# Kernel tuning notes

Measured on AMD Instinct MI355X. Metric: run time of the kernel, lower is better.

## Reference

```python
import jax, jax.numpy as jnp
import numpy as np
from jax import lax

B, CX, CZ, H, W = 8, 96, 96, 256, 256
HEADS = 4


def conv2d(x, w, groups=1, pad=0):
    return lax.conv_general_dilated(
        x, w, window_strides=(1, 1), padding=[(pad, pad), (pad, pad)],
        dimension_numbers=('NCHW', 'OIHW', 'NCHW'),
        feature_group_count=groups)


def setup_inputs() -> dict:
    key = jax.random.key(0)
    ks = jax.random.split(key, 8)
    def init_w(k, shape):
        fan_in = shape[1] * shape[2] * shape[3]
        bound = 1.0 / np.sqrt(fan_in)
        return jax.random.uniform(k, shape, jnp.float32, -bound, bound)
    return {
        'x': jax.random.normal(ks[0], (B, CX, H, W), jnp.float32),
        'z': jax.random.normal(ks[1], (B, CZ, H, W), jnp.float32),
        'kv_w1': init_w(ks[2], (2 * CZ, CZ, 1, 1)),
        'kv_w2': init_w(ks[3], (2 * CZ, 2, 3, 3)),   # grouped: groups=CZ, 2 in-ch per group
        'q_w1': init_w(ks[4], (CX, CX, 1, 1)),
        'q_w2': init_w(ks[5], (CX, 1, 3, 3)),        # depthwise: groups=CX
        'proj_w': init_w(ks[6], (CX, CX, 1, 1)),
        'temperature': jnp.ones((HEADS, 1, 1), jnp.float32),
    }


def _forward(x, z, kv_w1, kv_w2, q_w1, q_w2, proj_w, temperature):
    b, cx, h, w = x.shape
    cz = z.shape[1]
    hw = h * w
    kv = conv2d(conv2d(z, kv_w1), kv_w2, groups=cz, pad=1)   # [b, 2cz, h, w]
    q = conv2d(conv2d(x, q_w1), q_w2, groups=cx, pad=1)      # [b, cx, h, w]
    k, v = jnp.split(kv, 2, axis=1)
    # b (head c) h w -> b head c (h w)
    q = q.reshape(b, HEADS, cx // HEADS, hw)
    k = k.reshape(b, HEADS, cz // HEADS, hw)
    v = v.reshape(b, HEADS, cz // HEADS, hw)
    # L2 normalize along hw (torch F.normalize: x / max(||x||, eps))
    eps = 1e-12
    q = q / jnp.maximum(jnp.linalg.norm(q, axis=-1, keepdims=True), eps)
    k = k / jnp.maximum(jnp.linalg.norm(k, axis=-1, keepdims=True), eps)
    attn = jnp.einsum('bhcn,bhdn->bhcd', q, k) * temperature  # [b,head,cq,ck]
    attn = jax.nn.softmax(attn, axis=-1)
    out = jnp.einsum('bhcd,bhdn->bhcn', attn, v)              # [b,head,cq,hw]
    out = out.reshape(b, cx, h, w)
    return conv2d(out, proj_w)


def reference(x, z, kv_w1, kv_w2, q_w1, q_w2, proj_w, temperature):
    return _forward(x, z, kv_w1, kv_w2, q_w1, q_w2, proj_w, temperature)
```

## Files before the change

### kernel.cpp

```cpp
#include <hip/hip_runtime.h>
#include <math.h>

#define HWc 65536
#define Wd 256
#define Hd 256

typedef __attribute__((ext_vector_type(8))) short bf16x8;
typedef __attribute__((ext_vector_type(4))) float f32x4;

__device__ inline ushort f2bf_hi(float a) {
    uint u = __float_as_uint(a);
    uint r = u + 0x7FFFu + ((u >> 16) & 1u);
    return (ushort)(r >> 16);
}
__device__ inline float bf2f(ushort h) { return __uint_as_float((uint)h << 16); }

static const size_t SSQ_Q_OFF = 0;
static const size_t SSQ_K_OFF = 768;
static const size_t ATTN_OFF  = 1536;
static const size_t QWF_OFF   = 19968;
static const size_t KWF_OFF   = 29184;
static const size_t VWF_OFF   = 38400;
static const size_t W2F_OFF   = 47616;
static const size_t WS1_OFF   = 121344;

__global__ void prep_wfrag(const float* __restrict__ w, int woff,
                           ushort* __restrict__ wf) {
    int idx = blockIdx.x * 256 + threadIdx.x;
    if (idx < 9216) {
        int m = idx / 96, c = idx % 96;
        float val = w[(size_t)(woff + m) * 96 + c];
        ushort hi = f2bf_hi(val);
        float lo = val - bf2f(hi);
        wf[(c >> 5) * 3072 + m * 32 + (c & 31)] = hi;
        wf[9216 + (c >> 5) * 3072 + m * 32 + (c & 31)] = f2bf_hi(lo);
    }
}

__global__ __launch_bounds__(384) void conv1x1_mfma(
    const float* __restrict__ in, const ushort* __restrict__ wf,
    float* __restrict__ out)
{
    __shared__ ushort Ah[64][104];
    __shared__ ushort Al[64][104];
    int b = blockIdx.y;
    int px0 = blockIdx.x * 64;
    int t = threadIdx.x, lane = t & 63, wv = t >> 6;
    const float* inb = in + (size_t)b * 96 * HWc + px0;

    int m = 16 * wv + (lane & 15);
    int kbase = (lane >> 4) * 8;
    bf16x8 Bh[3], Bl[3];
#pragma unroll
    for (int ks = 0; ks < 3; ++ks) {
        Bh[ks] = *(const bf16x8*)&wf[ks * 3072 + m * 32 + kbase];
        Bl[ks] = *(const bf16x8*)&wf[9216 + ks * 3072 + m * 32 + kbase];
    }

#pragma unroll
    for (int rr = 0; rr < 4; ++rr) {
        int fi = rr * 384 + t;
        int c = fi >> 4;
        int p4 = (fi & 15) * 4;
        float4 v = *(const float4*)(inb + (size_t)c * HWc + p4);
        float vv[4] = {v.x, v.y, v.z, v.w};
#pragma unroll
        for (int e = 0; e < 4; ++e) {
            ushort hi = f2bf_hi(vv[e]);
            float lo = vv[e] - bf2f(hi);
            Ah[p4 + e][c] = hi;
            Al[p4 + e][c] = (ushort)f2bf_hi(lo);
        }
    }
    __syncthreads();

    f32x4 acc0 = {0.f, 0.f, 0.f, 0.f};
    f32x4 acc1 = {0.f, 0.f, 0.f, 0.f};
    f32x4 acc2 = {0.f, 0.f, 0.f, 0.f};
    f32x4 acc3 = {0.f, 0.f, 0.f, 0.f};
    int prow = lane & 15;

#pragma unroll
    for (int ks = 0; ks < 3; ++ks) {
        int ccol = ks * 32 + kbase;
#define DO_PT(PT, ACC)                                                         \
        {                                                                      \
            bf16x8 ah = *(const bf16x8*)&Ah[(PT) * 16 + prow][ccol];           \
            bf16x8 al = *(const bf16x8*)&Al[(PT) * 16 + prow][ccol];           \
            ACC = __builtin_amdgcn_mfma_f32_16x16x32_bf16(ah, Bh[ks], ACC, 0, 0, 0); \
            ACC = __builtin_amdgcn_mfma_f32_16x16x32_bf16(ah, Bl[ks], ACC, 0, 0, 0); \
            ACC = __builtin_amdgcn_mfma_f32_16x16x32_bf16(al, Bh[ks], ACC, 0, 0, 0); \
        }
        DO_PT(0, acc0) DO_PT(1, acc1) DO_PT(2, acc2) DO_PT(3, acc3)
#undef DO_PT
    }

    int pq = (lane >> 4) * 4;
    float* outm = out + (size_t)b * 96 * HWc + (size_t)m * HWc + px0 + pq;
    *(f32x4*)(outm + 0)  = acc0;
    *(f32x4*)(outm + 16) = acc1;
    *(f32x4*)(outm + 32) = acc2;
    *(f32x4*)(outm + 48) = acc3;
}

__global__ __launch_bounds__(256) void depthwise3x3_kernel(
    const float* __restrict__ in, const float* __restrict__ wq,
    float* __restrict__ out, float* __restrict__ ssq_q)
{
    __shared__ float red[4];
    int c = blockIdx.y, b = blockIdx.z;
    int t = threadIdx.x;
    int lane = t & 63;
    int xq = lane * 4;
    int yb = blockIdx.x * 32 + (t >> 6) * 8;

    const float* inc = in + ((size_t)(b * 96 + c)) * HWc;
    float* outc = out + ((size_t)(b * 96 + c)) * HWc;

    float w[9];
    const float* wp = wq + (size_t)c * 9;
#pragma unroll
    for (int i = 0; i < 9; ++i) w[i] = wp[i];

    float rows[3][6];

#define LOAD_ROW(yy, slot)                                                     \
    {                                                                          \
        float4 v_;                                                             \
        if ((unsigned)(yy) < (unsigned)Hd)                                     \
            v_ = *(const float4*)(inc + (size_t)(yy) * Wd + xq);               \
        else                                                                   \
            v_ = make_float4(0.f, 0.f, 0.f, 0.f);                              \
        float lw_ = __shfl_up(v_.w, 1, 64);                                    \
        float rx_ = __shfl_down(v_.x, 1, 64);                                  \
        rows[slot][0] = (lane > 0) ? lw_ : 0.f;                                \
        rows[slot][1] = v_.x; rows[slot][2] = v_.y;                            \
        rows[slot][3] = v_.z; rows[slot][4] = v_.w;                            \
        rows[slot][5] = (lane < 63) ? rx_ : 0.f;                               \
    }

    LOAD_ROW(yb - 1, 0);
    LOAD_ROW(yb, 1);

    float ssq = 0.f;
#pragma unroll
    for (int r = 0; r < 8; ++r) {
        LOAD_ROW(yb + r + 1, (r + 2) % 3);
        const float* ra = rows[r % 3];
        const float* rb = rows[(r + 1) % 3];
        const float* rc = rows[(r + 2) % 3];
        float a[4] = {0.f, 0.f, 0.f, 0.f};
#pragma unroll
        for (int dx = 0; dx < 3; ++dx)
#pragma unroll
            for (int px = 0; px < 4; ++px) {
                a[px] = fmaf(w[dx],     ra[px + dx], a[px]);
                a[px] = fmaf(w[3 + dx], rb[px + dx], a[px]);
                a[px] = fmaf(w[6 + dx], rc[px + dx], a[px]);
            }
        *(float4*)(outc + (size_t)(yb + r) * Wd + xq) = *(float4*)a;
#pragma unroll
        for (int px = 0; px < 4; ++px) ssq = fmaf(a[px], a[px], ssq);
    }
#undef LOAD_ROW

#pragma unroll
    for (int off = 32; off; off >>= 1) ssq += __shfl_down(ssq, off, 64);
    int wvi = t >> 6;
    if (lane == 0) red[wvi] = ssq;
    __syncthreads();
    if (t == 0) atomicAdd(&ssq_q[b * 96 + c], red[0] + red[1] + red[2] + red[3]);
}

#define CONV_PAIR(P, SS0, SS1)                                                 \
    {                                                                          \
        const float* m0 = midb + (size_t)(2 * (P)) * HWc;                      \
        const float* m1 = m0 + HWc;                                            \
        const float* wp_ = &wls[(P) * 36];                                     \
        float k0[4] = {0.f, 0.f, 0.f, 0.f};                                    \
        float k1[4] = {0.f, 0.f, 0.f, 0.f};                                    \
        _Pragma("unroll")                                                      \
        for (int dy = 0; dy < 3; ++dy) {                                       \
            int yy = y + dy - 1;                                               \
            if ((unsigned)yy < (unsigned)Hd) {                                 \
                _Pragma("unroll")                                              \
                for (int ic = 0; ic < 2; ++ic) {                               \
                    const float* base = (ic ? m1 : m0) + (size_t)yy * Wd;      \
                    float4 cv = *(const float4*)(base + x0);                   \
                    float rr[6];                                               \
                    rr[0] = (x0 > 0) ? base[x0 - 1] : 0.f;                     \
                    rr[1] = cv.x; rr[2] = cv.y; rr[3] = cv.z; rr[4] = cv.w;    \
                    rr[5] = (x0 < 252) ? base[x0 + 4] : 0.f;                   \
                    int wb_ = ic * 9 + dy * 3;                                 \
                    _Pragma("unroll")                                          \
                    for (int px = 0; px < 4; ++px) {                           \
                        _Pragma("unroll")                                      \
                        for (int dx = 0; dx < 3; ++dx) {                       \
                            k0[px] = fmaf(wp_[wb_ + dx],      rr[px + dx], k0[px]); \
                            k1[px] = fmaf(wp_[18 + wb_ + dx], rr[px + dx], k1[px]); \
                        }                                                      \
                    }                                                          \
                }                                                              \
            }                                                                  \
        }                                                                      \
        _Pragma("unroll")                                                      \
        for (int px = 0; px < 4; ++px) {                                       \
            SS0 = fmaf(k0[px], k0[px], SS0);                                   \
            SS1 = fmaf(k1[px], k1[px], SS1);                                   \
        }                                                                      \
        *(float4*)&ks[2 * (P)][l32 * 4]     = *(float4*)k0;                    \
        *(float4*)&ks[2 * (P) + 1][l32 * 4] = *(float4*)k1;                    \
    }

__global__ __launch_bounds__(256) void k_logits_kernel(
    const float* __restrict__ mid, const float* __restrict__ w2,
    const float* __restrict__ qg, float* __restrict__ attn_raw,
    float* __restrict__ ssq_k)
{
    __shared__ float qs[24][132];
    __shared__ float ks[24][132];
    __shared__ float wls[24 * 18];

    int bx = blockIdx.x;
    int yt = bx >> 1, xh = bx & 1;
    int h = blockIdx.y, b = blockIdx.z;
    int xbase = xh * 128;
    int t = threadIdx.x, lane = t & 63, wvi = t >> 6;
    int hi = lane >> 5, l32 = lane & 31;
    int i0 = (lane >> 3) * 3, j0 = (lane & 7) * 3;

    const float* midb = mid + ((size_t)b * 96 + h * 24) * HWc;
    const float* qb   = qg  + ((size_t)b * 96 + h * 24) * HWc;

    if (t < 108)
        *(float4*)&wls[4 * t] = *(const float4*)(w2 + (size_t)h * 432 + 4 * t);

    int pA = 2 * wvi + hi;
    int pB = 8 + 2 * wvi + hi;
    int x0 = xbase + l32 * 4;

    float acc[3][3];
#pragma unroll
    for (int a = 0; a < 3; ++a)
#pragma unroll
        for (int c2 = 0; c2 < 3; ++c2) acc[a][c2] = 0.f;
    float ssqA0 = 0.f, ssqA1 = 0.f, ssqB0 = 0.f, ssqB1 = 0.f;

    __syncthreads();

    for (int r = 0; r < 8; ++r) {
        int y = yt * 8 + r;
        __syncthreads();

        {
            const float* qrow = qb + (size_t)y * Wd + xbase;
            int fi = t;
            *(float4*)&qs[fi >> 5][(fi & 31) * 4] =
                *(const float4*)(qrow + (size_t)(fi >> 5) * HWc + (fi & 31) * 4);
            fi = t + 256;
            *(float4*)&qs[fi >> 5][(fi & 31) * 4] =
                *(const float4*)(qrow + (size_t)(fi >> 5) * HWc + (fi & 31) * 4);
        }
        CONV_PAIR(pA, ssqA0, ssqA1);
        if (t < 128) {
            CONV_PAIR(pB, ssqB0, ssqB1);
        } else {
            const float* qrow = qb + (size_t)y * Wd + xbase;
            int fi = 512 + (t - 128);
            *(float4*)&qs[fi >> 5][(fi & 31) * 4] =
                *(const float4*)(qrow + (size_t)(fi >> 5) * HWc + (fi & 31) * 4);
            fi = 640 + (t - 128);
            *(float4*)&qs[fi >> 5][(fi & 31) * 4] =
                *(const float4*)(qrow + (size_t)(fi >> 5) * HWc + (fi & 31) * 4);
        }
        __syncthreads();

        int n0 = wvi * 32;
#pragma unroll 4
        for (int nn = 0; nn < 8; ++nn) {
            int n = n0 + nn * 4;
            float4 q0v = *(const float4*)&qs[i0][n];
            float4 q1v = *(const float4*)&qs[i0 + 1][n];
            float4 q2v = *(const float4*)&qs[i0 + 2][n];
            float4 k0v = *(const float4*)&ks[j0][n];
            float4 k1v = *(const float4*)&ks[j0 + 1][n];
            float4 k2v = *(const float4*)&ks[j0 + 2][n];
            acc[0][0] += q0v.x*k0v.x + q0v.y*k0v.y + q0v.z*k0v.z + q0v.w*k0v.w;
            acc[0][1] += q0v.x*k1v.x + q0v.y*k1v.y + q0v.z*k1v.z + q0v.w*k1v.w;
            acc[0][2] += q0v.x*k2v.x + q0v.y*k2v.y + q0v.z*k2v.z + q0v.w*k2v.w;
            acc[1][0] += q1v.x*k0v.x + q1v.y*k0v.y + q1v.z*k0v.z + q1v.w*k0v.w;
            acc[1][1] += q1v.x*k1v.x + q1v.y*k1v.y + q1v.z*k1v.z + q1v.w*k1v.w;
            acc[1][2] += q1v.x*k2v.x + q1v.y*k2v.y + q1v.z*k2v.z + q1v.w*k2v.w;
            acc[2][0] += q2v.x*k0v.x + q2v.y*k0v.y + q2v.z*k0v.z + q2v.w*k0v.w;
            acc[2][1] += q2v.x*k1v.x + q2v.y*k1v.y + q2v.z*k1v.z + q2v.w*k1v.w;
            acc[2][2] += q2v.x*k2v.x + q2v.y*k2v.y + q2v.z*k2v.z + q2v.w*k2v.w;
        }
    }

    {
        float s0 = ssqA0, s1 = ssqA1;
#pragma unroll
        for (int off = 16; off; off >>= 1) {
            s0 += __shfl_down(s0, off, 32);
            s1 += __shfl_down(s1, off, 32);
        }
        if (l32 == 0) {
            atomicAdd(&ssq_k[b * 96 + h * 24 + 2 * pA],     s0);
            atomicAdd(&ssq_k[b * 96 + h * 24 + 2 * pA + 1], s1);
        }
    }
    if (t < 128) {
        float s0 = ssqB0, s1 = ssqB1;
#pragma unroll
        for (int off = 16; off; off >>= 1) {
            s0 += __shfl_down(s0, off, 32);
            s1 += __shfl_down(s1, off, 32);
        }
        if (l32 == 0) {
            atomicAdd(&ssq_k[b * 96 + h * 24 + 2 * pB],     s0);
            atomicAdd(&ssq_k[b * 96 + h * 24 + 2 * pB + 1], s1);
        }
    }

    __syncthreads();
    float* redbuf = &qs[0][0];
#pragma unroll
    for (int a = 0; a < 3; ++a)
#pragma unroll
        for (int c2 = 0; c2 < 3; ++c2)
            redbuf[wvi * 576 + (i0 + a) * 24 + (j0 + c2)] = acc[a][c2];
    __syncthreads();
    for (int p_ = t; p_ < 576; p_ += 256) {
        float s4 = redbuf[p_] + redbuf[576 + p_] + redbuf[1152 + p_] + redbuf[1728 + p_];
        atomicAdd(&attn_raw[((size_t)b * 4 + h) * 576 + p_], s4);
    }
}

__global__ __launch_bounds__(256) void softmax_fold_kernel(
    const float* __restrict__ attn_raw,
    const float* __restrict__ ssq_q, const float* __restrict__ ssq_k,
    const float* __restrict__ temp, const float* __restrict__ projw,
    ushort* __restrict__ W2F)
{
    __shared__ float s[24][25];
    __shared__ float rq[24], rk[24];
    int h = blockIdx.x, b = blockIdx.y;
    int t = threadIdx.x;

    if (t < 24) {
        rq[t] = 1.f / fmaxf(sqrtf(ssq_q[b * 96 + h * 24 + t]), 1e-12f);
        rk[t] = 1.f / fmaxf(sqrtf(ssq_k[b * 96 + h * 24 + t]), 1e-12f);
    }
    __syncthreads();
    float T = temp[h];
    for (int p = t; p < 576; p += 256) {
        int i = p / 24, j = p % 24;
        s[i][j] = attn_raw[(size_t)(b * 4 + h) * 576 + p] * T * rq[i] * rk[j];
    }
    __syncthreads();
    if (t < 24) {
        float m = -1e30f;
#pragma unroll
        for (int j = 0; j < 24; ++j) m = fmaxf(m, s[t][j]);
        float sum = 0.f;
#pragma unroll
        for (int j = 0; j < 24; ++j) { float e = __expf(s[t][j] - m); s[t][j] = e; sum += e; }
        float inv = 1.f / sum;
#pragma unroll
        for (int j = 0; j < 24; ++j) s[t][j] *= inv;
    }
    __syncthreads();
    ushort* wfb = W2F + (size_t)b * 18432;
    for (int m_ = t; m_ < 96 * 24; m_ += 256) {
        int d = m_ % 24, co = m_ / 24;
        float acc = 0.f;
#pragma unroll
        for (int c = 0; c < 24; ++c)
            acc += projw[co * 96 + h * 24 + c] * s[c][d];
        int dv = h * 24 + d;
        int ks = dv >> 5, kk = dv & 31;
        ushort hi = f2bf_hi(acc);
        float lo = acc - bf2f(hi);
        wfb[ks * 3072 + co * 32 + kk] = hi;
        wfb[9216 + ks * 3072 + co * 32 + kk] = f2bf_hi(lo);
    }
}

__global__ __launch_bounds__(384) void v_proj_mfma(
    const float* __restrict__ mid, const float* __restrict__ w2,
    const ushort* __restrict__ W2F, float* __restrict__ out)
{
    __shared__ ushort Ah[64][128];
    __shared__ ushort Al[64][128];
    __shared__ float wls[1728];

    int bx = blockIdx.x, b = blockIdx.y;
    int y = bx >> 2;
    int x0 = (bx & 3) * 64;
    int t = threadIdx.x, lane = t & 63, wv = t >> 6;
    const float* midb = mid + (size_t)b * 96 * HWc;

    for (int i = t; i < 432; i += 384)
        *(float4*)&wls[4 * i] = *(const float4*)(w2 + 96 * 18 + 4 * i);

    int m = 16 * wv + (lane & 15);
    int kbase = (lane >> 4) * 8;
    const ushort* wfb = W2F + (size_t)b * 18432;
    bf16x8 Bh[3], Bl[3];
#pragma unroll
    for (int ks = 0; ks < 3; ++ks) {
        Bh[ks] = *(const bf16x8*)&wfb[ks * 3072 + m * 32 + kbase];
        Bl[ks] = *(const bf16x8*)&wfb[9216 + ks * 3072 + m * 32 + kbase];
    }
    __syncthreads();

    {
        int p = t >> 3;
        int xl = (t & 7) * 8;
        int xg = x0 + xl;
        const float* m0 = midb + (size_t)(2 * p) * HWc;
        const float* m1 = m0 + HWc;
        const float* wp_ = &wls[p * 36];
        float k0[8] = {0.f,0.f,0.f,0.f,0.f,0.f,0.f,0.f};
        float k1[8] = {0.f,0.f,0.f,0.f,0.f,0.f,0.f,0.f};
#pragma unroll
        for (int dy = 0; dy < 3; ++dy) {
            int yy = y + dy - 1;
            if ((unsigned)yy < (unsigned)Hd) {
#pragma unroll
                for (int ic = 0; ic < 2; ++ic) {
                    const float* base = (ic ? m1 : m0) + (size_t)yy * Wd;
                    float4 a = *(const float4*)(base + xg);
                    float4 b2 = *(const float4*)(base + xg + 4);
                    float rr[10];
                    rr[0] = (xg > 0) ? base[xg - 1] : 0.f;
                    rr[1] = a.x; rr[2] = a.y; rr[3] = a.z; rr[4] = a.w;
                    rr[5] = b2.x; rr[6] = b2.y; rr[7] = b2.z; rr[8] = b2.w;
                    rr[9] = (xg + 8 < 256) ? base[xg + 8] : 0.f;
                    int wb_ = ic * 9 + dy * 3;
#pragma unroll
                    for (int px = 0; px < 8; ++px) {
#pragma unroll
                        for (int dx = 0; dx < 3; ++dx) {
                            k0[px] = fmaf(wp_[wb_ + dx],      rr[px + dx], k0[px]);
                            k1[px] = fmaf(wp_[18 + wb_ + dx], rr[px + dx], k1[px]);
                        }
                    }
                }
            }
        }
#pragma unroll
        for (int px = 0; px < 8; ++px) {
            int row = xl + px;
            uint sw = (uint)(row & 7) << 4;
            uint off = ((uint)(4 * p)) ^ sw;
            ushort h0 = f2bf_hi(k0[px]);
            ushort h1 = f2bf_hi(k1[px]);
            float l0 = k0[px] - bf2f(h0);
            float l1 = k1[px] - bf2f(h1);
            *(uint*)((char*)&Ah[row][0] + off) = (uint)h0 | ((uint)h1 << 16);
            *(uint*)((char*)&Al[row][0] + off) =
                (uint)f2bf_hi(l0) | ((uint)f2bf_hi(l1) << 16);
        }
    }
    __syncthreads();

    f32x4 acc0 = {0.f, 0.f, 0.f, 0.f};
    f32x4 acc1 = {0.f, 0.f, 0.f, 0.f};
    f32x4 acc2 = {0.f, 0.f, 0.f, 0.f};
    f32x4 acc3 = {0.f, 0.f, 0.f, 0.f};
    int prow = lane & 15;

#pragma unroll
    for (int ks = 0; ks < 3; ++ks) {
        uint cbyte = (uint)(ks * 32 + kbase) * 2;
#define DO_PT(PT, ACC)                                                         \
        {                                                                      \
            int row = (PT) * 16 + prow;                                        \
            uint sw = (uint)(row & 7) << 4;                                    \
            bf16x8 ah = *(const bf16x8*)((char*)&Ah[row][0] + (cbyte ^ sw));   \
            bf16x8 al = *(const bf16x8*)((char*)&Al[row][0] + (cbyte ^ sw));   \
            ACC = __builtin_amdgcn_mfma_f32_16x16x32_bf16(ah, Bh[ks], ACC, 0, 0, 0); \
            ACC = __builtin_amdgcn_mfma_f32_16x16x32_bf16(ah, Bl[ks], ACC, 0, 0, 0); \
            ACC = __builtin_amdgcn_mfma_f32_16x16x32_bf16(al, Bh[ks], ACC, 0, 0, 0); \
        }
        DO_PT(0, acc0) DO_PT(1, acc1) DO_PT(2, acc2) DO_PT(3, acc3)
#undef DO_PT
    }

    int pq = (lane >> 4) * 4;
    float* outm = out + (size_t)b * 96 * HWc + (size_t)m * HWc
                + (size_t)y * Wd + x0 + pq;
    *(f32x4*)(outm + 0)  = acc0;
    *(f32x4*)(outm + 16) = acc1;
    *(f32x4*)(outm + 32) = acc2;
    *(f32x4*)(outm + 48) = acc3;
}

extern "C" void kernel_launch(void* const* d_in, const int* in_sizes, int n_in,
                              void* d_out, int out_size, void* d_ws, size_t ws_size,
                              hipStream_t stream) {
    const float* x     = (const float*)d_in[0];
    const float* z     = (const float*)d_in[1];
    const float* kvw1  = (const float*)d_in[2];
    const float* kvw2  = (const float*)d_in[3];
    const float* qw1   = (const float*)d_in[4];
    const float* qw2   = (const float*)d_in[5];
    const float* projw = (const float*)d_in[6];
    const float* temp  = (const float*)d_in[7];
    float* out = (float*)d_out;
    float* ws  = (float*)d_ws;
    (void)in_sizes; (void)n_in; (void)out_size; (void)ws_size;

    float* ssq_q = ws + SSQ_Q_OFF;
    float* ssq_k = ws + SSQ_K_OFF;
    float* attn  = ws + ATTN_OFF;
    ushort* qwf  = (ushort*)(ws + QWF_OFF);
    ushort* kwf  = (ushort*)(ws + KWF_OFF);
    ushort* vwf  = (ushort*)(ws + VWF_OFF);
    ushort* w2f  = (ushort*)(ws + W2F_OFF);
    float* ws1   = ws + WS1_OFF;

    hipMemsetAsync(ws, 0, (768 + 768 + 18432) * sizeof(float), stream);

    prep_wfrag<<<dim3(36), 256, 0, stream>>>(qw1, 0, qwf);
    prep_wfrag<<<dim3(36), 256, 0, stream>>>(kvw1, 0, kwf);
    prep_wfrag<<<dim3(36), 256, 0, stream>>>(kvw1, 96, vwf);

    conv1x1_mfma<<<dim3(1024, 8), 384, 0, stream>>>(x, qwf, ws1);
    depthwise3x3_kernel<<<dim3(8, 96, 8), 256, 0, stream>>>(ws1, qw2, out, ssq_q);

    conv1x1_mfma<<<dim3(1024, 8), 384, 0, stream>>>(z, kwf, ws1);
    k_logits_kernel<<<dim3(64, 4, 8), 256, 0, stream>>>(ws1, kvw2, out, attn, ssq_k);

    softmax_fold_kernel<<<dim3(4, 8), 256, 0, stream>>>(attn, ssq_q, ssq_k, temp, projw, w2f);

    conv1x1_mfma<<<dim3(1024, 8), 384, 0, stream>>>(z, vwf, ws1);
    v_proj_mfma<<<dim3(1024, 8), 384, 0, stream>>>(ws1, kvw2, w2f, out);
}
```

Baseline: 737.8 us.

## Compute q·k logits with split-bf16 MFMA instead of scalar FMA

The 24x24 q·k^T logits accumulation in k_logits_kernel now runs on matrix cores. q and k tiles are stored in shared memory as hi/lo bf16 pairs padded to 32 rows, and three bf16 MFMA products (hh, hl, lh) stand in for the fp32 dot products. This removes the scalar FMA inner loop and the cross-wave shared-memory reduction, and each wave atomically adds its tile directly. The cost is extra conversion work when staging q and k, padded rows that do wasted MFMA work, and slightly lower precision than full fp32.

```diff
diff --git a/kernel.cpp b/kernel.cpp
--- a/kernel.cpp
+++ b/kernel.cpp
@@ -14,6 +14,21 @@
     return (ushort)(r >> 16);
 }
 __device__ inline float bf2f(ushort h) { return __uint_as_float((uint)h << 16); }
+
+__device__ inline void store_hl4(ushort* hp, ushort* lp, const float* v) {
+    ushort hs[4], ls[4];
+#pragma unroll
+    for (int e = 0; e < 4; ++e) {
+        hs[e] = f2bf_hi(v[e]);
+        ls[e] = f2bf_hi(v[e] - bf2f(hs[e]));
+    }
+    uint2 hv = make_uint2((uint)hs[0] | ((uint)hs[1] << 16),
+                          (uint)hs[2] | ((uint)hs[3] << 16));
+    uint2 lv = make_uint2((uint)ls[0] | ((uint)ls[1] << 16),
+                          (uint)ls[2] | ((uint)ls[3] << 16));
+    *(uint2*)hp = hv;
+    *(uint2*)lp = lv;
+}
 
 static const size_t SSQ_Q_OFF = 0;
 static const size_t SSQ_K_OFF = 768;
@@ -186,11 +201,11 @@
                 _Pragma("unroll")                                              \
                 for (int ic = 0; ic < 2; ++ic) {                               \
                     const float* base = (ic ? m1 : m0) + (size_t)yy * Wd;      \
-                    float4 cv = *(const float4*)(base + x0);                   \
+                    float4 cv = *(const float4*)(base + xg);                   \
                     float rr[6];                                               \
-                    rr[0] = (x0 > 0) ? base[x0 - 1] : 0.f;                     \
+                    rr[0] = (xg > 0) ? base[xg - 1] : 0.f;                     \
                     rr[1] = cv.x; rr[2] = cv.y; rr[3] = cv.z; rr[4] = cv.w;    \
-                    rr[5] = (x0 < 252) ? base[x0 + 4] : 0.f;                   \
+                    rr[5] = (xg < 252) ? base[xg + 4] : 0.f;                   \
                     int wb_ = ic * 9 + dy * 3;                                 \
                     _Pragma("unroll")                                          \
                     for (int px = 0; px < 4; ++px) {                           \
@@ -208,8 +223,17 @@
             SS0 = fmaf(k0[px], k0[px], SS0);                                   \
             SS1 = fmaf(k1[px], k1[px], SS1);                                   \
         }                                                                      \
-        *(float4*)&ks[2 * (P)][l32 * 4]     = *(float4*)k0;                    \
-        *(float4*)&ks[2 * (P) + 1][l32 * 4] = *(float4*)k1;                    \
+        store_hl4(&fr[2][2 * (P)][x0l],     &fr[3][2 * (P)][x0l],     k0);     \
+        store_hl4(&fr[2][2 * (P) + 1][x0l], &fr[3][2 * (P) + 1][x0l], k1);     \
+    }
+
+#define ST_Q(FI)                                                               \
+    {                                                                          \
+        int ch = (FI) >> 5;                                                    \
+        int xo = ((FI) & 31) * 4;                                              \
+        float4 v = *(const float4*)(qrow + (size_t)ch * HWc + xo);             \
+        float vv[4] = {v.x, v.y, v.z, v.w};                                    \
+        store_hl4(&fr[0][ch][xo], &fr[1][ch][xo], vv);                         \
     }
 
 __global__ __launch_bounds__(256) void k_logits_kernel(
@@ -217,8 +241,7 @@
     const float* __restrict__ qg, float* __restrict__ attn_raw,
     float* __restrict__ ssq_k)
 {
-    __shared__ float qs[24][132];
-    __shared__ float ks[24][132];
+    __shared__ ushort fr[4][32][136];
     __shared__ float wls[24 * 18];
 
     int bx = blockIdx.x;
@@ -227,23 +250,26 @@
     int xbase = xh * 128;
     int t = threadIdx.x, lane = t & 63, wvi = t >> 6;
     int hi = lane >> 5, l32 = lane & 31;
-    int i0 = (lane >> 3) * 3, j0 = (lane & 7) * 3;
 
     const float* midb = mid + ((size_t)b * 96 + h * 24) * HWc;
     const float* qb   = qg  + ((size_t)b * 96 + h * 24) * HWc;
 
     if (t < 108)
         *(float4*)&wls[4 * t] = *(const float4*)(w2 + (size_t)h * 432 + 4 * t);
+    for (int i = t; i < 2176; i += 256) {
+        int plane = i / 544, idx = i % 544;
+        ((uint*)&fr[plane][24][0])[idx] = 0;
+    }
 
     int pA = 2 * wvi + hi;
     int pB = 8 + 2 * wvi + hi;
-    int x0 = xbase + l32 * 4;
-
-    float acc[3][3];
-#pragma unroll
-    for (int a = 0; a < 3; ++a)
-#pragma unroll
-        for (int c2 = 0; c2 < 3; ++c2) acc[a][c2] = 0.f;
+    int x0l = l32 * 4;
+    int xg = xbase + x0l;
+
+    int mi = wvi >> 1, nj = wvi & 1;
+    int prow16 = lane & 15, kb = (lane >> 4) * 8;
+
+    f32x4 acc = {0.f, 0.f, 0.f, 0.f};
     float ssqA0 = 0.f, ssqA1 = 0.f, ssqB0 = 0.f, ssqB1 = 0.f;
 
     __syncthreads();
@@ -255,11 +281,9 @@
         {
             const float* qrow = qb + (size_t)y * Wd + xbase;
             int fi = t;
-            *(float4*)&qs[fi >> 5][(fi & 31) * 4] =
-                *(const float4*)(qrow + (size_t)(fi >> 5) * HWc + (fi & 31) * 4);
+            ST_Q(fi);
             fi = t + 256;
-            *(float4*)&qs[fi >> 5][(fi & 31) * 4] =
-                *(const float4*)(qrow + (size_t)(fi >> 5) * HWc + (fi & 31) * 4);
+            ST_Q(fi);
         }
         CONV_PAIR(pA, ssqA0, ssqA1);
         if (t < 128) {
@@ -267,33 +291,22 @@
         } else {
             const float* qrow = qb + (size_t)y * Wd + xbase;
             int fi = 512 + (t - 128);
-            *(float4*)&qs[fi >> 5][(fi & 31) * 4] =
-                *(const float4*)(qrow + (size_t)(fi >> 5) * HWc + (fi & 31) * 4);
+            ST_Q(fi);
             fi = 640 + (t - 128);
-            *(float4*)&qs[fi >> 5][(fi & 31) * 4] =
-                *(const float4*)(qrow + (size_t)(fi >> 5) * HWc + (fi & 31) * 4);
+            ST_Q(fi);
         }
         __syncthreads();
 
-        int n0 = wvi * 32;
-#pragma unroll 4
-        for (int nn = 0; nn < 8; ++nn) {
-            int n = n0 + nn * 4;
-            float4 q0v = *(const float4*)&qs[i0][n];
-            float4 q1v = *(const float4*)&qs[i0 + 1][n];
-            float4 q2v = *(const float4*)&qs[i0 + 2][n];
-            float4 k0v = *(const float4*)&ks[j0][n];
-            float4 k1v = *(const float4*)&ks[j0 + 1][n];
-            float4 k2v = *(const float4*)&ks[j0 + 2][n];
-            acc[0][0] += q0v.x*k0v.x + q0v.y*k0v.y + q0v.z*k0v.z + q0v.w*k0v.w;
-            acc[0][1] += q0v.x*k1v.x + q0v.y*k1v.y + q0v.z*k1v.z + q0v.w*k1v.w;
-            acc[0][2] += q0v.x*k2v.x + q0v.y*k2v.y + q0v.z*k2v.z + q0v.w*k2v.w;
-            acc[1][0] += q1v.x*k0v.x + q1v.y*k0v.y + q1v.z*k0v.z + q1v.w*k0v.w;
-            acc[1][1] += q1v.x*k1v.x + q1v.y*k1v.y + q1v.z*k1v.z + q1v.w*k1v.w;
-            acc[1][2] += q1v.x*k2v.x + q1v.y*k2v.y + q1v.z*k2v.z + q1v.w*k2v.w;
-            acc[2][0] += q2v.x*k0v.x + q2v.y*k0v.y + q2v.z*k0v.z + q2v.w*k0v.w;
-            acc[2][1] += q2v.x*k1v.x + q2v.y*k1v.y + q2v.z*k1v.z + q2v.w*k1v.w;
-            acc[2][2] += q2v.x*k2v.x + q2v.y*k2v.y + q2v.z*k2v.z + q2v.w*k2v.w;
+#pragma unroll
+        for (int ks2 = 0; ks2 < 4; ++ks2) {
+            int col = ks2 * 32 + kb;
+            bf16x8 ah = *(const bf16x8*)&fr[0][mi * 16 + prow16][col];
+            bf16x8 al = *(const bf16x8*)&fr[1][mi * 16 + prow16][col];
+            bf16x8 bh = *(const bf16x8*)&fr[2][nj * 16 + prow16][col];
+            bf16x8 bl = *(const bf16x8*)&fr[3][nj * 16 + prow16][col];
+            acc = __builtin_amdgcn_mfma_f32_16x16x32_bf16(ah, bh, acc, 0, 0, 0);
+            acc = __builtin_amdgcn_mfma_f32_16x16x32_bf16(ah, bl, acc, 0, 0, 0);
+            acc = __builtin_amdgcn_mfma_f32_16x16x32_bf16(al, bh, acc, 0, 0, 0);
         }
     }
 
@@ -322,17 +335,15 @@
         }
     }
 
-    __syncthreads();
-    float* redbuf = &qs[0][0];
-#pragma unroll
-    for (int a = 0; a < 3; ++a)
-#pragma unroll
-        for (int c2 = 0; c2 < 3; ++c2)
-            redbuf[wvi * 576 + (i0 + a) * 24 + (j0 + c2)] = acc[a][c2];
-    __syncthreads();
-    for (int p_ = t; p_ < 576; p_ += 256) {
-        float s4 = redbuf[p_] + redbuf[576 + p_] + redbuf[1152 + p_] + redbuf[1728 + p_];
-        atomicAdd(&attn_raw[((size_t)b * 4 + h) * 576 + p_], s4);
+    int jcol = nj * 16 + (lane & 15);
+    if (jcol < 24) {
+        float* dst = attn_raw + ((size_t)b * 4 + h) * 576;
+#pragma unroll
+        for (int rg = 0; rg < 4; ++rg) {
+            int irow = mi * 16 + (lane >> 4) * 4 + rg;
+            if (irow < 24)
+                atomicAdd(&dst[irow * 24 + jcol], acc[rg]);
+        }
     }
 }
 
```

Result: no change. 735.8 us (-0.3%).
